# Kernel tuning notes

Measured on AMD Instinct MI355X. Metric: run time of the kernel, lower is better.

Reference implementation:

```python
import jax, jax.numpy as jnp
import numpy as np
from jax import lax

N_Q = 4          # kernel_size**2 for Q_conv(kernel_size=2)
DIM = 16         # 2**N_Q statevector dimension
N_LAYERS = 3

# --- static circuit constants -------------------------------------------

def _cnot_np(c, t):
    # PennyLane convention: wire 0 is the most-significant bit.
    M = np.zeros((DIM, DIM), np.complex64)
    for s in range(DIM):
        s2 = s ^ (1 << (N_Q - 1 - t)) if (s >> (N_Q - 1 - c)) & 1 else s
        M[s2, s] = 1.0
    return jnp.asarray(M)

# StronglyEntanglingLayers: layer l uses range r = l % (n_wires-1) + 1
_CNOTS = {r: [_cnot_np(i, (i + r) % N_Q) for i in range(N_Q)] for r in (1, 2, 3)}

_ZDIAG = jnp.asarray(np.array(
    [[1.0 - 2.0 * ((s >> (N_Q - 1 - w)) & 1) for w in range(N_Q)] for s in range(DIM)],
    np.float32))  # (16, 4): diag of PauliZ on each wire


def _rot(p):
    # qml.Rot(phi, theta, omega) = RZ(omega) RY(theta) RZ(phi)
    phi, th, om = p[0], p[1], p[2]
    c, s = jnp.cos(th / 2), jnp.sin(th / 2)
    r0 = jnp.stack([jnp.exp(-1j * (phi + om) / 2) * c, -jnp.exp(1j * (phi - om) / 2) * s])
    r1 = jnp.stack([jnp.exp(-1j * (phi - om) / 2) * s, jnp.exp(1j * (phi + om) / 2) * c])
    return jnp.stack([r0, r1]).astype(jnp.complex64)


def _circuit_unitary(qw):
    # qw: (3, 4, 3). One StronglyEntanglingLayers block of 3 layers,
    # which the qnode applies n_layers=3 times with the SAME weights.
    U = jnp.eye(DIM, dtype=jnp.complex64)
    for l in range(N_LAYERS):
        L = _rot(qw[l, 0])
        for q in range(1, N_Q):
            L = jnp.kron(L, _rot(qw[l, q]))
        for C in _CNOTS[l + 1]:
            L = C @ L
        U = L @ U
    return U @ U @ U


def _quanv(x, qw):
    # x: (B, 1, 44, 44); k = stride = 2 -> non-overlapping 2x2 patches.
    B, H = x.shape[0], x.shape[-1]
    o = H // 2  # 22
    patches = x.reshape(B, o, 2, o, 2).transpose(0, 1, 3, 2, 4).reshape(-1, 4)
    # AngleEmbedding (RX) on |0000> gives a product state.
    a = jnp.cos(patches / 2).astype(jnp.complex64)
    b = (-1j * jnp.sin(patches / 2)).astype(jnp.complex64)
    w = jnp.stack([a, b], axis=-1)  # (N, 4, 2)
    psi0 = jnp.einsum('na,nb,nc,nd->nabcd', w[:, 0], w[:, 1], w[:, 2], w[:, 3]).reshape(-1, DIM)
    psi = psi0 @ _circuit_unitary(qw).T  # (N, 16)
    probs = psi.real ** 2 + psi.imag ** 2
    e = probs @ _ZDIAG  # (N, 4) expvals of PauliZ per wire
    return e.reshape(B, o * o, N_Q).transpose(0, 2, 1).reshape(B, N_Q, o, o).astype(x.dtype)


def _conv(x, w, b, stride):
    y = lax.conv_general_dilated(x, w, (stride, stride), 'VALID',
                                 dimension_numbers=('NCHW', 'OIHW', 'NCHW'))
    return y + b[None, :, None, None]


def _maxpool(x, k, s):
    return lax.reduce_window(x, -jnp.inf, lax.max, (1, 1, k, k), (1, 1, s, s), 'VALID')


def setup_inputs() -> dict:
    key = jax.random.key(0)
    ks = jax.random.split(key, 18)
    B = 256
    f32 = jnp.float32
    return {
        'x': jax.random.normal(ks[0], (B, 1, 186, 186), f32),
        'conv1_w': jax.random.normal(ks[1], (1, 1, 8, 8), f32) * 0.1,
        'conv1_b': jax.random.normal(ks[2], (1,), f32) * 0.05,
        'q_w': jax.random.uniform(ks[3], (3, 4, 3), f32, 0.0, 2.0 * np.pi),
        'conv2_w': jax.random.normal(ks[4], (32, 4, 4, 4), f32) * 0.1,
        'conv2_b': jax.random.normal(ks[5], (32,), f32) * 0.05,
        'conv3_w': jax.random.normal(ks[6], (64, 32, 4, 4), f32) * 0.05,
        'conv3_b': jax.random.normal(ks[7], (64,), f32) * 0.05,
        'conv4_w': jax.random.normal(ks[8], (128, 64, 4, 4), f32) * 0.03,
        'conv4_b': jax.random.normal(ks[9], (128,), f32) * 0.05,
        'fc1_w': jax.random.normal(ks[10], (128, 3200), f32) * 0.02,
        'fc1_b': jax.random.normal(ks[11], (128,), f32) * 0.05,
        'fc2_w': jax.random.normal(ks[12], (64, 128), f32) * 0.09,
        'fc2_b': jax.random.normal(ks[13], (64,), f32) * 0.05,
        'fc3_w': jax.random.normal(ks[14], (16, 64), f32) * 0.12,
        'fc3_b': jax.random.normal(ks[15], (16,), f32) * 0.05,
        'fc4_w': jax.random.normal(ks[16], (2, 16), f32) * 0.25,
        'fc4_b': jax.random.normal(ks[17], (2,), f32) * 0.05,
    }


def reference(x, conv1_w, conv1_b, q_w, conv2_w, conv2_b, conv3_w, conv3_b,
              conv4_w, conv4_b, fc1_w, fc1_b, fc2_w, fc2_b, fc3_w, fc3_b,
              fc4_w, fc4_b):
    h = _maxpool(jnp.tanh(_conv(x, conv1_w, conv1_b, 2)), 4, 2) * (np.pi / 2)
    h = jax.nn.relu(_quanv(h, q_w))                       # (B, 4, 22, 22)
    h = _maxpool(jax.nn.relu(_conv(h, conv2_w, conv2_b, 1)), 4, 1)
    h = _maxpool(jax.nn.relu(_conv(h, conv3_w, conv3_b, 1)), 2, 1)
    h = jax.nn.relu(_conv(h, conv4_w, conv4_b, 2))        # (B, 128, 5, 5)
    h = h.reshape(h.shape[0], -1)
    h = jax.nn.relu(h @ fc1_w.T + fc1_b)   # dropout: eval mode = identity
    h = jax.nn.relu(h @ fc2_w.T + fc2_b)
    h = jax.nn.relu(h @ fc3_w.T + fc3_b)
    return jax.nn.log_softmax(h @ fc4_w.T + fc4_b, axis=1)
```

## Files before the change

### kernel.cpp

```cpp
#include <hip/hip_runtime.h>
#include <hip/hip_bf16.h>
#include <math.h>


__device__ __forceinline__ float2 cmul(float2 a, float2 b) {
    return make_float2(a.x * b.x - a.y * b.y, a.x * b.y + a.y * b.x);
}
__device__ __forceinline__ float2 cfma(float2 a, float2 b, float2 acc) {
    acc.x += a.x * b.x - a.y * b.y;
    acc.y += a.x * b.y + a.y * b.x;
    return acc;
}

__global__ __launch_bounds__(256) void k_build_V(const float* __restrict__ qw,
                                                 float2* __restrict__ Vout) {
    __shared__ float2 rot[3][4][2][2];
    __shared__ float2 L[16][16];
    __shared__ float2 U[16][16];
    __shared__ float2 T[16][16];

    int tid = threadIdx.x;
    if (tid < 12) {
        int l = tid >> 2, q = tid & 3;
        float phi = qw[(l * 4 + q) * 3 + 0];
        float th  = qw[(l * 4 + q) * 3 + 1];
        float om  = qw[(l * 4 + q) * 3 + 2];
        float c, s;
        sincosf(0.5f * th, &s, &c);
        float sa, ca, sb, cb;
        sincosf(0.5f * (phi + om), &sa, &ca);
        sincosf(0.5f * (phi - om), &sb, &cb);
        rot[l][q][0][0] = make_float2( ca * c, -sa * c);
        rot[l][q][0][1] = make_float2(-cb * s, -sb * s);
        rot[l][q][1][0] = make_float2( cb * s, -sb * s);
        rot[l][q][1][1] = make_float2( ca * c,  sa * c);
    }
    int s = tid >> 4, t = tid & 15;
    U[s][t] = make_float2((s == t) ? 1.f : 0.f, 0.f);
    __syncthreads();

    for (int l = 0; l < 3; ++l) {
        int r = l + 1;
        int ss = s;
        for (int i = 3; i >= 0; --i) {
            int c_ = i, t_ = (i + r) & 3;
            if ((ss >> (3 - c_)) & 1) ss ^= 1 << (3 - t_);
        }
        float2 v = make_float2(1.f, 0.f);
        #pragma unroll
        for (int q = 0; q < 4; ++q) {
            int bs = (ss >> (3 - q)) & 1;
            int bt = (t  >> (3 - q)) & 1;
            v = cmul(v, rot[l][q][bs][bt]);
        }
        L[s][t] = v;
        __syncthreads();
        float2 acc = make_float2(0.f, 0.f);
        #pragma unroll
        for (int k = 0; k < 16; ++k) acc = cfma(L[s][k], U[k][t], acc);
        T[s][t] = acc;
        __syncthreads();
        U[s][t] = T[s][t];
        __syncthreads();
    }
    float2 acc = make_float2(0.f, 0.f);
    #pragma unroll
    for (int k = 0; k < 16; ++k) acc = cfma(U[s][k], U[k][t], acc);
    T[s][t] = acc;
    __syncthreads();
    acc = make_float2(0.f, 0.f);
    #pragma unroll
    for (int k = 0; k < 16; ++k) acc = cfma(T[s][k], U[k][t], acc);
    int pc = __popc(t) & 3;
    float2 v;
    if      (pc == 0) v = acc;
    else if (pc == 1) v = make_float2( acc.y, -acc.x);
    else if (pc == 2) v = make_float2(-acc.x, -acc.y);
    else              v = make_float2(-acc.y,  acc.x);
    Vout[s * 16 + t] = v;
}

__global__ __launch_bounds__(256) void k_wtrans(const float* __restrict__ w3,
                                                const float* __restrict__ w4,
                                                float* __restrict__ wt3,
                                                float* __restrict__ wt4) {
    int idx = blockIdx.x * 256 + threadIdx.x;
    if (idx < 32768) {
        int oc = idx & 63, tap = (idx >> 6) & 15, ic = idx >> 10;
        wt3[idx] = w3[oc * 512 + ic * 16 + tap];
    } else {
        int o = idx - 32768;
        int oc = o & 127, tap = (o >> 7) & 15, ic = o >> 11;
        wt4[o] = w4[oc * 1024 + ic * 16 + tap];
    }
}

__global__ __launch_bounds__(256) void k_conv1d(const float* __restrict__ x,
                                                const float* __restrict__ w,
                                                const float* __restrict__ bias,
                                                float* __restrict__ y) {
    int idx = blockIdx.x * 256 + threadIdx.x;
    int j = idx % 90;
    int t = idx / 90;
    int i = t % 90;
    int b = t / 90;
    const float* xb = x + b * 34596 + (2 * i) * 186 + 2 * j;
    float acc = bias[0];
    #pragma unroll
    for (int u = 0; u < 8; ++u) {
        const float* rp = xb + u * 186;
        float2 p0 = *(const float2*)(rp + 0);
        float2 p1 = *(const float2*)(rp + 2);
        float2 p2 = *(const float2*)(rp + 4);
        float2 p3 = *(const float2*)(rp + 6);
        acc = fmaf(w[u * 8 + 0], p0.x, acc);
        acc = fmaf(w[u * 8 + 1], p0.y, acc);
        acc = fmaf(w[u * 8 + 2], p1.x, acc);
        acc = fmaf(w[u * 8 + 3], p1.y, acc);
        acc = fmaf(w[u * 8 + 4], p2.x, acc);
        acc = fmaf(w[u * 8 + 5], p2.y, acc);
        acc = fmaf(w[u * 8 + 6], p3.x, acc);
        acc = fmaf(w[u * 8 + 7], p3.y, acc);
    }
    y[idx] = tanhf(acc);
}

__global__ __launch_bounds__(256) void k_quanvp(const float* __restrict__ y,
                                                const float2* __restrict__ Vg,
                                                float* __restrict__ o) {
    __shared__ float2 V[256];
    V[threadIdx.x] = Vg[threadIdx.x];
    __syncthreads();

    int idx = blockIdx.x * 256 + threadIdx.x;
    int j = idx % 22;
    int t = idx / 22;
    int i = t % 22;
    int b = t / 22;

    const float* yb = y + b * 8100 + (4 * i) * 90 + 4 * j;
    float ra[6], rb[6];
    #pragma unroll
    for (int r = 0; r < 6; ++r) {
        const float* rp = yb + r * 90;
        float2 p0 = *(const float2*)(rp);
        float2 p1 = *(const float2*)(rp + 2);
        float2 p2 = *(const float2*)(rp + 4);
        float m01 = fmaxf(p0.x, p0.y);
        float m23 = fmaxf(p1.x, p1.y);
        float m45 = fmaxf(p2.x, p2.y);
        ra[r] = fmaxf(m01, m23);
        rb[r] = fmaxf(m23, m45);
    }
    const float S = 1.57079632679489662f;
    float a0 = S * fmaxf(fmaxf(ra[0], ra[1]), fmaxf(ra[2], ra[3]));
    float a1 = S * fmaxf(fmaxf(rb[0], rb[1]), fmaxf(rb[2], rb[3]));
    float a2 = S * fmaxf(fmaxf(ra[2], ra[3]), fmaxf(ra[4], ra[5]));
    float a3 = S * fmaxf(fmaxf(rb[2], rb[3]), fmaxf(rb[4], rb[5]));

    float cs[4], sn[4];
    sincosf(0.5f * a0, &sn[0], &cs[0]);
    sincosf(0.5f * a1, &sn[1], &cs[1]);
    sincosf(0.5f * a2, &sn[2], &cs[2]);
    sincosf(0.5f * a3, &sn[3], &cs[3]);

    float c[16];
    #pragma unroll
    for (int tt = 0; tt < 16; ++tt) {
        c[tt] = ((tt & 8) ? sn[0] : cs[0]) * ((tt & 4) ? sn[1] : cs[1]) *
                ((tt & 2) ? sn[2] : cs[2]) * ((tt & 1) ? sn[3] : cs[3]);
    }

    float e0 = 0.f, e1 = 0.f, e2 = 0.f, e3 = 0.f;
    #pragma unroll
    for (int s = 0; s < 16; ++s) {
        float re = 0.f, im = 0.f;
        #pragma unroll
        for (int tt = 0; tt < 16; ++tt) {
            float2 v = V[s * 16 + tt];
            re = fmaf(v.x, c[tt], re);
            im = fmaf(v.y, c[tt], im);
        }
        float pr = re * re + im * im;
        e0 += (s & 8) ? -pr : pr;
        e1 += (s & 4) ? -pr : pr;
        e2 += (s & 2) ? -pr : pr;
        e3 += (s & 1) ? -pr : pr;
    }
    float* ob = o + b * (4 * 484) + i * 22 + j;
    ob[0]    = fmaxf(e0, 0.f);
    ob[484]  = fmaxf(e1, 0.f);
    ob[968]  = fmaxf(e2, 0.f);
    ob[1452] = fmaxf(e3, 0.f);
}

__global__ __launch_bounds__(640) void k_conv2t(const float* __restrict__ x,
                                                const float* __restrict__ w,
                                                const float* __restrict__ bias,
                                                float* __restrict__ y) {
    __shared__ float Xs[4 * 22 * 28];
    __shared__ float Ws[32 * 68];
    int b = blockIdx.x;
    int tid = threadIdx.x;

    const float* xb = x + b * 1936;
    for (int k = tid; k < 1936; k += 640) {
        int ic = k / 484, rem = k % 484;
        int r = rem / 22, c = rem % 22;
        Xs[ic * 616 + r * 28 + c] = xb[k];
    }
    for (int k = tid; k < 2048; k += 640) {
        Ws[(k >> 6) * 68 + (k & 63)] = w[k];
    }
    __syncthreads();

    if (tid < 608) {
        int oc = tid / 19, i = tid % 19;
        float acc[19];
        float bv = bias[oc];
        #pragma unroll
        for (int j = 0; j < 19; ++j) acc[j] = bv;
        const float* wr = &Ws[oc * 68];
        #pragma unroll
        for (int ic = 0; ic < 4; ++ic) {
            #pragma unroll
            for (int u = 0; u < 4; ++u) {
                const float* rp = &Xs[ic * 616 + (i + u) * 28];
                float xr[22];
                #pragma unroll
                for (int k = 0; k < 5; ++k)
                    *(float4*)&xr[4 * k] = *(const float4*)(rp + 4 * k);
                *(float2*)&xr[20] = *(const float2*)(rp + 20);
                float4 wv = *(const float4*)(wr + ic * 16 + u * 4);
                #pragma unroll
                for (int j = 0; j < 19; ++j) {
                    acc[j] = fmaf(wv.x, xr[j],     acc[j]);
                    acc[j] = fmaf(wv.y, xr[j + 1], acc[j]);
                    acc[j] = fmaf(wv.z, xr[j + 2], acc[j]);
                    acc[j] = fmaf(wv.w, xr[j + 3], acc[j]);
                }
            }
        }
        float* yp = y + b * 11552 + oc * 361 + i * 19;
        #pragma unroll
        for (int j = 0; j < 19; ++j) yp[j] = fmaxf(acc[j], 0.f);
    }
}

__global__ __launch_bounds__(256) void k_pool2(const float* __restrict__ x,
                                               float* __restrict__ y) {
    int idx = blockIdx.x * 256 + threadIdx.x;
    int j = idx % 16;
    int t = idx / 16;
    int i = t % 16;
    int c = t / 16;
    const float* xb = x + c * 361 + i * 19 + j;
    float m = -INFINITY;
    #pragma unroll
    for (int u = 0; u < 4; ++u)
        #pragma unroll
        for (int v = 0; v < 4; ++v)
            m = fmaxf(m, xb[u * 19 + v]);
    y[idx] = m;
}

__global__ __launch_bounds__(448) void k_conv3y(const float* __restrict__ x,
                                                const float* __restrict__ wt3,
                                                const float* __restrict__ bias,
                                                float* __restrict__ y) {
    __shared__ float Xs[32 * 200];
    __shared__ float Rs[112 * 57];
    int bid = blockIdx.x;
    int b = bid >> 1, h = bid & 1;
    int r0 = h * 7;
    int nr = 7 - h;
    int tid = threadIdx.x;

    const float* xb = x + b * 8192 + r0 * 16;
    #pragma unroll
    for (int it = 0; it < 3; ++it) {
        int k = it * 448 + tid;
        if (k < 1280) {
            int ic = k / 40, rem = k % 40;
            int r = rem >> 2, c4 = rem & 3;
            if (r0 + r < 16) {
                float4 v = *(const float4*)(xb + ic * 256 + r * 16 + c4 * 4);
                *(float4*)(&Xs[ic * 200 + r * 20 + c4 * 4]) = v;
            }
        }
    }
    __syncthreads();

    int kg = tid / 112;
    int t2 = tid - kg * 112;
    int ocq = t2 & 15, il = t2 >> 4;
    int oc0 = ocq * 4;

    float acc[4][13];
    #pragma unroll
    for (int o = 0; o < 4; ++o)
        #pragma unroll
        for (int j = 0; j < 13; ++j) acc[o][j] = 0.f;

    const float* wb = wt3 + kg * 8192 + oc0;
    #pragma unroll 1
    for (int k = 0; k < 8; ++k) {
        const float* wp = wb + k * 1024;
        const float* xc = &Xs[(kg * 8 + k) * 200 + il * 20];
        #pragma unroll
        for (int u = 0; u < 4; ++u) {
            float xr[16];
            const float* rp = xc + u * 20;
            #pragma unroll
            for (int kk = 0; kk < 4; ++kk)
                *(float4*)&xr[4 * kk] = *(const float4*)(rp + 4 * kk);
            #pragma unroll
            for (int v = 0; v < 4; ++v) {
                float4 wv = *(const float4*)(wp + (u * 4 + v) * 64);
                #pragma unroll
                for (int j = 0; j < 13; ++j) {
                    acc[0][j] = fmaf(wv.x, xr[j + v], acc[0][j]);
                    acc[1][j] = fmaf(wv.y, xr[j + v], acc[1][j]);
                    acc[2][j] = fmaf(wv.z, xr[j + v], acc[2][j]);
                    acc[3][j] = fmaf(wv.w, xr[j + v], acc[3][j]);
                }
            }
        }
    }

    #pragma unroll
    for (int g = 1; g < 4; ++g) {
        __syncthreads();
        if (kg == g) {
            float* rp = &Rs[t2 * 57];
            #pragma unroll
            for (int o = 0; o < 4; ++o)
                #pragma unroll
                for (int j = 0; j < 13; ++j) rp[o * 13 + j] = acc[o][j];
        }
        __syncthreads();
        if (kg == 0) {
            const float* rp = &Rs[t2 * 57];
            #pragma unroll
            for (int o = 0; o < 4; ++o)
                #pragma unroll
                for (int j = 0; j < 13; ++j)
                    acc[o][j] += rp[o * 13 + j];
        }
    }

    if (kg == 0 && il < nr) {
        float* yp = y + b * 10816 + oc0 * 169 + (r0 + il) * 13;
        #pragma unroll
        for (int o = 0; o < 4; ++o) {
            float bv = bias[oc0 + o];
            #pragma unroll
            for (int j = 0; j < 13; ++j)
                yp[o * 169 + j] = fmaxf(acc[o][j] + bv, 0.f);
        }
    }
}

__global__ __launch_bounds__(640) void k_conv4y(const float* __restrict__ x3,
                                                const float* __restrict__ wt4,
                                                float* __restrict__ part) {
    __shared__ float Xs[32 * 144];
    __shared__ float Rs[160 * 21];
    int bid = blockIdx.x;
    int b = bid >> 1, kq = bid & 1;
    int tid = threadIdx.x;

    const float* gb = x3 + b * 10816 + kq * 32 * 169;
    for (int k = tid; k < 4608; k += 640) {
        int ic = k / 144, rc = k % 144;
        int r = rc / 12, c = rc % 12;
        const float* g = gb + ic * 169 + r * 13 + c;
        Xs[k] = fmaxf(fmaxf(g[0], g[1]), fmaxf(g[13], g[14]));
    }
    __syncthreads();

    int kg = tid / 160;
    int t2 = tid - kg * 160;
    int ocq = t2 & 31, i = t2 >> 5;
    int oc0 = ocq * 4;

    float acc[4][5];
    #pragma unroll
    for (int o = 0; o < 4; ++o)
        #pragma unroll
        for (int j = 0; j < 5; ++j) acc[o][j] = 0.f;

    const float* wb = wt4 + (kq * 32 + kg * 8) * 2048 + oc0;
    #pragma unroll 1
    for (int k = 0; k < 8; ++k) {
        const float* wp = wb + k * 2048;
        const float* xc = &Xs[(kg * 8 + k) * 144];
        #pragma unroll
        for (int u = 0; u < 4; ++u) {
            const float* rp = xc + (2 * i + u) * 12;
            float xr[12];
            #pragma unroll
            for (int kk = 0; kk < 3; ++kk)
                *(float4*)&xr[4 * kk] = *(const float4*)(rp + 4 * kk);
            #pragma unroll
            for (int v = 0; v < 4; ++v) {
                float4 wv = *(const float4*)(wp + (u * 4 + v) * 128);
                #pragma unroll
                for (int j = 0; j < 5; ++j) {
                    float xv = xr[2 * j + v];
                    acc[0][j] = fmaf(wv.x, xv, acc[0][j]);
                    acc[1][j] = fmaf(wv.y, xv, acc[1][j]);
                    acc[2][j] = fmaf(wv.z, xv, acc[2][j]);
                    acc[3][j] = fmaf(wv.w, xv, acc[3][j]);
                }
            }
        }
    }

    #pragma unroll
    for (int g = 1; g < 4; ++g) {
        __syncthreads();
        if (kg == g) {
            float* rp = &Rs[t2 * 21];
            #pragma unroll
            for (int o = 0; o < 4; ++o)
                #pragma unroll
                for (int j = 0; j < 5; ++j) rp[o * 5 + j] = acc[o][j];
        }
        __syncthreads();
        if (kg == 0) {
            const float* rp = &Rs[t2 * 21];
            #pragma unroll
            for (int o = 0; o < 4; ++o)
                #pragma unroll
                for (int j = 0; j < 5; ++j) acc[o][j] += rp[o * 5 + j];
        }
    }

    if (kg == 0) {
        float* pp = part + kq * 819200 + b * 3200 + oc0 * 25 + i * 5;
        #pragma unroll
        for (int o = 0; o < 4; ++o)
            #pragma unroll
            for (int j = 0; j < 5; ++j) pp[o * 25 + j] = acc[o][j];
    }
}

__global__ __launch_bounds__(256) void k_fc1f(const float* __restrict__ part,
                                              const float* __restrict__ w,
                                              const float* __restrict__ b4,
                                              const float* __restrict__ bias,
                                              float* __restrict__ y) {
    __shared__ float Ls[4][32][65];
    int bid = blockIdx.x;
    int ig = bid >> 2, ocg = bid & 3;
    int imgB = ig * 4, ocB = ocg * 32;
    int tid = threadIdx.x, lane = tid & 63, wv = tid >> 6;
    int ocW = ocB + wv * 8;

    float acc[8][4];
    #pragma unroll
    for (int o = 0; o < 8; ++o)
        #pragma unroll
        for (int m = 0; m < 4; ++m) acc[o][m] = 0.f;

    for (int it = 0; it < 25; ++it) {
        int k = it * 128 + lane * 2;
        float ba = b4[k / 25];
        float bb = b4[(k + 1) / 25];
        float2 xv[4];
        #pragma unroll
        for (int m = 0; m < 4; ++m) {
            int base = (imgB + m) * 3200 + k;
            float2 p0 = *(const float2*)&part[base];
            float2 p1 = *(const float2*)&part[base + 819200];
            xv[m].x = fmaxf(p0.x + p1.x + ba, 0.f);
            xv[m].y = fmaxf(p0.y + p1.y + bb, 0.f);
        }
        #pragma unroll
        for (int o = 0; o < 8; ++o) {
            float2 wvv = *(const float2*)&w[(ocW + o) * 3200 + k];
            #pragma unroll
            for (int m = 0; m < 4; ++m) {
                acc[o][m] = fmaf(wvv.x, xv[m].x, acc[o][m]);
                acc[o][m] = fmaf(wvv.y, xv[m].y, acc[o][m]);
            }
        }
    }
    #pragma unroll
    for (int o = 0; o < 8; ++o)
        #pragma unroll
        for (int m = 0; m < 4; ++m)
            Ls[wv][o * 4 + m][lane] = acc[o][m];
    __syncthreads();

    if (tid < 128) {
        int w2 = tid >> 5, r = tid & 31;
        const float* p = Ls[w2][r];
        float s = 0.f;
        #pragma unroll
        for (int c = 0; c < 64; ++c) s += p[c];
        int o = r >> 2, m = r & 3;
        int oc = ocB + w2 * 8 + o;
        y[(imgB + m) * 128 + oc] = fmaxf(s + bias[oc], 0.f);
    }
}

__global__ __launch_bounds__(64) void k_fc_tail(const float* __restrict__ x,
                                                const float* __restrict__ w2,
                                                const float* __restrict__ b2,
                                                const float* __restrict__ w3,
                                                const float* __restrict__ b3,
                                                const float* __restrict__ w4,
                                                const float* __restrict__ b4,
                                                float* __restrict__ out) {
    __shared__ float xs[128], h2[64], h3[16];
    int img = blockIdx.x;
    int lane = threadIdx.x;

    *(float2*)&xs[lane * 2] = *(const float2*)&x[img * 128 + lane * 2];
    __syncthreads();

    float a = b2[lane];
    const float4* wp = (const float4*)&w2[lane * 128];
    const float4* xp = (const float4*)xs;
    #pragma unroll
    for (int k = 0; k < 32; ++k) {
        float4 wv = wp[k], xv = xp[k];
        a = fmaf(wv.x, xv.x, a);
        a = fmaf(wv.y, xv.y, a);
        a = fmaf(wv.z, xv.z, a);
        a = fmaf(wv.w, xv.w, a);
    }
    h2[lane] = fmaxf(a, 0.f);
    __syncthreads();

    if (lane < 16) {
        float a3 = b3[lane];
        const float4* w3p = (const float4*)&w3[lane * 64];
        const float4* h2p = (const float4*)h2;
        #pragma unroll
        for (int k = 0; k < 16; ++k) {
            float4 wv = w3p[k], xv = h2p[k];
            a3 = fmaf(wv.x, xv.x, a3);
            a3 = fmaf(wv.y, xv.y, a3);
            a3 = fmaf(wv.z, xv.z, a3);
            a3 = fmaf(wv.w, xv.w, a3);
        }
        h3[lane] = fmaxf(a3, 0.f);
    }
    __syncthreads();

    if (lane == 0) {
        float z0 = b4[0], z1 = b4[1];
        #pragma unroll
        for (int k = 0; k < 16; ++k) {
            z0 = fmaf(w4[k],      h3[k], z0);
            z1 = fmaf(w4[16 + k], h3[k], z1);
        }
        float m = fmaxf(z0, z1);
        float lse = m + logf(expf(z0 - m) + expf(z1 - m));
        out[img * 2 + 0] = z0 - lse;
        out[img * 2 + 1] = z1 - lse;
    }
}

extern "C" void kernel_launch(void* const* d_in, const int* in_sizes, int n_in,
                              void* d_out, int out_size, void* d_ws, size_t ws_size,
                              hipStream_t stream) {
    const float* x       = (const float*)d_in[0];
    const float* conv1_w = (const float*)d_in[1];
    const float* conv1_b = (const float*)d_in[2];
    const float* q_w     = (const float*)d_in[3];
    const float* conv2_w = (const float*)d_in[4];
    const float* conv2_b = (const float*)d_in[5];
    const float* conv3_w = (const float*)d_in[6];
    const float* conv3_b = (const float*)d_in[7];
    const float* conv4_w = (const float*)d_in[8];
    const float* conv4_b = (const float*)d_in[9];
    const float* fc1_w   = (const float*)d_in[10];
    const float* fc1_b   = (const float*)d_in[11];
    const float* fc2_w   = (const float*)d_in[12];
    const float* fc2_b   = (const float*)d_in[13];
    const float* fc3_w   = (const float*)d_in[14];
    const float* fc3_b   = (const float*)d_in[15];
    const float* fc4_w   = (const float*)d_in[16];
    const float* fc4_b   = (const float*)d_in[17];
    float* out = (float*)d_out;

    char* ws = (char*)d_ws;
    float2* V  = (float2*)ws;
    float* A   = (float*)(ws + 4096);
    float* B   = (float*)(ws + 12587008);
    float* WT3 = (float*)(ws + 21499904);
    float* WT4 = (float*)(ws + 21639168);

    k_build_V<<<1, 256, 0, stream>>>(q_w, V);
    k_wtrans<<<640, 256, 0, stream>>>(conv3_w, conv4_w, WT3, WT4);
    k_conv1d<<<8100, 256, 0, stream>>>(x, conv1_w, conv1_b, A);
    k_quanvp<<<484, 256, 0, stream>>>(A, V, B);
    k_conv2t<<<256, 640, 0, stream>>>(B, conv2_w, conv2_b, A);
    k_pool2<<<8192, 256, 0, stream>>>(A, B);
    k_conv3y<<<512, 448, 0, stream>>>(B, WT3, conv3_b, A);
    k_conv4y<<<512, 640, 0, stream>>>(A, WT4, B);
    k_fc1f<<<256, 256, 0, stream>>>(B, fc1_w, conv4_b, fc1_b, A);
    k_fc_tail<<<256, 64, 0, stream>>>(A, fc2_w, fc2_b, fc3_w, fc3_b,
                                      fc4_w, fc4_b, out);
}
```

Baseline: 162.0 us.

## Fuse conv1, tanh and maxpool into the quanvolution kernel

Result: no change. 159.3 us (-1.6%).

```diff
diff --git a/kernel.cpp b/kernel.cpp
--- a/kernel.cpp
+++ b/kernel.cpp
@@ -95,39 +95,11 @@
     }
 }
 
-__global__ __launch_bounds__(256) void k_conv1d(const float* __restrict__ x,
-                                                const float* __restrict__ w,
-                                                const float* __restrict__ bias,
-                                                float* __restrict__ y) {
-    int idx = blockIdx.x * 256 + threadIdx.x;
-    int j = idx % 90;
-    int t = idx / 90;
-    int i = t % 90;
-    int b = t / 90;
-    const float* xb = x + b * 34596 + (2 * i) * 186 + 2 * j;
-    float acc = bias[0];
-    #pragma unroll
-    for (int u = 0; u < 8; ++u) {
-        const float* rp = xb + u * 186;
-        float2 p0 = *(const float2*)(rp + 0);
-        float2 p1 = *(const float2*)(rp + 2);
-        float2 p2 = *(const float2*)(rp + 4);
-        float2 p3 = *(const float2*)(rp + 6);
-        acc = fmaf(w[u * 8 + 0], p0.x, acc);
-        acc = fmaf(w[u * 8 + 1], p0.y, acc);
-        acc = fmaf(w[u * 8 + 2], p1.x, acc);
-        acc = fmaf(w[u * 8 + 3], p1.y, acc);
-        acc = fmaf(w[u * 8 + 4], p2.x, acc);
-        acc = fmaf(w[u * 8 + 5], p2.y, acc);
-        acc = fmaf(w[u * 8 + 6], p3.x, acc);
-        acc = fmaf(w[u * 8 + 7], p3.y, acc);
-    }
-    y[idx] = tanhf(acc);
-}
-
-__global__ __launch_bounds__(256) void k_quanvp(const float* __restrict__ y,
-                                                const float2* __restrict__ Vg,
-                                                float* __restrict__ o) {
+__global__ __launch_bounds__(256) void k_cq(const float* __restrict__ x,
+                                            const float* __restrict__ w,
+                                            const float* __restrict__ bias,
+                                            const float2* __restrict__ Vg,
+                                            float* __restrict__ o) {
     __shared__ float2 V[256];
     V[threadIdx.x] = Vg[threadIdx.x];
     __syncthreads();
@@ -138,20 +110,50 @@
     int i = t % 22;
     int b = t / 22;
 
-    const float* yb = y + b * 8100 + (4 * i) * 90 + 4 * j;
+    const float* xb = x + b * 34596 + (8 * i) * 186 + 8 * j;
+    float bv = bias[0];
+
+    float win[8][18];
+    #pragma unroll
+    for (int u = 0; u < 8; ++u)
+        #pragma unroll
+        for (int k2 = 0; k2 < 9; ++k2)
+            *(float2*)&win[u][2 * k2] = *(const float2*)(xb + u * 186 + 2 * k2);
+
     float ra[6], rb[6];
     #pragma unroll
     for (int r = 0; r < 6; ++r) {
-        const float* rp = yb + r * 90;
-        float2 p0 = *(const float2*)(rp);
-        float2 p1 = *(const float2*)(rp + 2);
-        float2 p2 = *(const float2*)(rp + 4);
-        float m01 = fmaxf(p0.x, p0.y);
-        float m23 = fmaxf(p1.x, p1.y);
-        float m45 = fmaxf(p2.x, p2.y);
+        if (r > 0) {
+            #pragma unroll
+            for (int nn = 0; nn < 2; ++nn) {
+                const int row = 2 * r + 6 + nn;
+                const int slot = row & 7;
+                #pragma unroll
+                for (int k2 = 0; k2 < 9; ++k2)
+                    *(float2*)&win[slot][2 * k2] =
+                        *(const float2*)(xb + row * 186 + 2 * k2);
+            }
+        }
+        float cl[6];
+        #pragma unroll
+        for (int c = 0; c < 6; ++c) {
+            float acc = bv;
+            #pragma unroll
+            for (int u = 0; u < 8; ++u) {
+                const int srow = (2 * r + u) & 7;
+                #pragma unroll
+                for (int v = 0; v < 8; ++v)
+                    acc = fmaf(w[u * 8 + v], win[srow][2 * c + v], acc);
+            }
+            cl[c] = tanhf(acc);
+        }
+        float m01 = fmaxf(cl[0], cl[1]);
+        float m23 = fmaxf(cl[2], cl[3]);
+        float m45 = fmaxf(cl[4], cl[5]);
         ra[r] = fmaxf(m01, m23);
         rb[r] = fmaxf(m23, m45);
     }
+
     const float S = 1.57079632679489662f;
     float a0 = S * fmaxf(fmaxf(ra[0], ra[1]), fmaxf(ra[2], ra[3]));
     float a1 = S * fmaxf(fmaxf(rb[0], rb[1]), fmaxf(rb[2], rb[3]));
@@ -597,8 +599,7 @@
 
     k_build_V<<<1, 256, 0, stream>>>(q_w, V);
     k_wtrans<<<640, 256, 0, stream>>>(conv3_w, conv4_w, WT3, WT4);
-    k_conv1d<<<8100, 256, 0, stream>>>(x, conv1_w, conv1_b, A);
-    k_quanvp<<<484, 256, 0, stream>>>(A, V, B);
+    k_cq<<<484, 256, 0, stream>>>(x, conv1_w, conv1_b, V, B);
     k_conv2t<<<256, 640, 0, stream>>>(B, conv2_w, conv2_b, A);
     k_pool2<<<8192, 256, 0, stream>>>(A, B);
     k_conv3y<<<512, 448, 0, stream>>>(B, WT3, conv3_b, A);
```
